# Optimization experiments

Hardware: AMD Instinct MI355X
Metric: run time of the kernel (lower is better)

The kernel has to match this reference:

```python
import jax, jax.numpy as jnp
import numpy as np

B, S, D, H = 2, 2048, 1024, 16
HD = D // H
E, K = 4, 2              # n_routed_experts, num_experts_per_tok
HID = int(4.0 * D)       # mlp_ratio * d_model
ALPHA = 0.01             # aux (load-balance) loss coefficient
EPS = 1e-5


def _ln(x, g, b):
    m = jnp.mean(x, -1, keepdims=True)
    v = jnp.var(x, -1, keepdims=True)
    return (x - m) * jax.lax.rsqrt(v + EPS) * g + b


def setup_inputs() -> dict:
    key = jax.random.key(0)
    ks = jax.random.split(key, 9)
    s = 0.02
    f32 = jnp.float32
    return {
        "x": jax.random.normal(ks[0], (B, S, D), f32),
        "ln1_g": jnp.ones((D,), f32), "ln1_b": jnp.zeros((D,), f32),
        "Wqkv": jax.random.normal(ks[1], (3 * D, D), f32) * s,
        "bqkv": jnp.zeros((3 * D,), f32),
        "Wo": jax.random.normal(ks[2], (D, D), f32) * s,
        "bo": jnp.zeros((D,), f32),
        "ln2_g": jnp.ones((D,), f32), "ln2_b": jnp.zeros((D,), f32),
        "Wg": jax.random.normal(ks[3], (E, D), f32) * s,            # router (no bias)
        "We_up": jax.random.normal(ks[4], (E, HID, D), f32) * s,
        "be_up": jnp.zeros((E, HID), f32),
        "We_down": jax.random.normal(ks[5], (E, D, HID), f32) * s,
        "be_down": jnp.zeros((E, D), f32),
        "Ws_up": jax.random.normal(ks[6], (HID, D), f32) * s,       # shared expert
        "bs_up": jnp.zeros((HID,), f32),
        "Ws_down": jax.random.normal(ks[7], (D, HID), f32) * s,
        "bs_down": jnp.zeros((D,), f32),
    }


def reference(x, ln1_g, ln1_b, Wqkv, bqkv, Wo, bo, ln2_g, ln2_b,
              Wg, We_up, be_up, We_down, be_down,
              Ws_up, bs_up, Ws_down, bs_down):
    # ---- causal multi-head self-attention (pre-LN) ----
    h = _ln(x, ln1_g, ln1_b)
    qkv = h @ Wqkv.T + bqkv                              # [B,S,3D]
    q, k, v = jnp.split(qkv, 3, axis=-1)
    to_heads = lambda t: t.reshape(B, S, H, HD).transpose(0, 2, 1, 3)
    q, k, v = to_heads(q), to_heads(k), to_heads(v)       # [B,H,S,HD]
    scores = jnp.einsum('bhqd,bhkd->bhqk', q, k) / np.float32(np.sqrt(HD))
    causal = jnp.tril(jnp.ones((S, S), bool))
    scores = jnp.where(causal, scores, jnp.float32(-1e9))
    attn = jax.nn.softmax(scores, axis=-1)
    o = jnp.einsum('bhqk,bhkd->bhqd', attn, v)
    o = o.transpose(0, 2, 1, 3).reshape(B, S, D)
    x = x + (o @ Wo.T + bo)                               # residual 1

    # ---- MoE feed-forward (pre-LN) ----
    T = B * S
    h2 = _ln(x, ln2_g, ln2_b).reshape(T, D)
    logits = h2 @ Wg.T                                    # [T,E]
    probs = jax.nn.softmax(logits, axis=-1)
    topw, topi = jax.lax.top_k(probs, K)                  # [T,K]
    topw = topw / jnp.sum(topw, -1, keepdims=True)        # renormalize top-k

    # dense expert evaluation (faithful math; kernel target is the sparse dispatch)
    up = jax.nn.gelu(jnp.einsum('td,ehd->eth', h2, We_up) + be_up[:, None, :])
    eo = jnp.einsum('eth,edh->etd', up, We_down) + be_down[:, None, :]  # [E,T,D]
    gathered = eo[topi.T, jnp.arange(T)[None, :]]         # [K,T,D]
    y = jnp.einsum('kt,ktd->td', topw.T, gathered)        # combine

    # shared expert (always-on)
    y = y + (jax.nn.gelu(h2 @ Ws_up.T + bs_up) @ Ws_down.T + bs_down)

    # load-balancing auxiliary loss (switch-style)
    assign = jax.nn.one_hot(topi, E, dtype=probs.dtype).sum(1)  # [T,E]
    fi = jnp.mean(assign, 0) / K                          # fraction routed to each expert
    Pi = jnp.mean(probs, 0)                               # mean router prob
    aux = ALPHA * E * jnp.sum(fi * Pi)

    x = x + y.reshape(B, S, D)                            # residual 2
    return aux, x
```

## Files before the change

kernel.cpp:

```cpp
#include <hip/hip_runtime.h>
#include <hip/hip_bf16.h>

#define T_TOK 4096
#define DIM   1024
#define NHEAD 16
#define HDIM  64
#define SEQ   2048
#define NEXP  4
#define HIDD  4096
#define QS    66

typedef short bf16x8 __attribute__((ext_vector_type(8)));
typedef float f32x4  __attribute__((ext_vector_type(4)));

enum { GF_GELU = 1, GF_RESID = 2, GF_SCALE = 4, GF_ACCUM = 8 };

__device__ inline unsigned short f2bf(float f) {
  union { float f; unsigned u; } v; v.f = f;
  unsigned r = v.u + 0x7FFFu + ((v.u >> 16) & 1u);
  return (unsigned short)(r >> 16);
}
__device__ inline int pack2(float a, float b) {
  return (int)((unsigned)f2bf(a) | ((unsigned)f2bf(b) << 16));
}
__device__ inline float gelu_f(float x) {
  float u = 1.5957691216057308f * x * (1.0f + 0.044715f * x * x);
  float w = __expf(u);
  return x - x * __builtin_amdgcn_rcpf(w + 1.0f);
}
__device__ inline void gld_lds16(const unsigned short* g, unsigned short* l) {
  __builtin_amdgcn_global_load_lds(
      (const __attribute__((address_space(1))) void*)g,
      (__attribute__((address_space(3))) void*)l, 16, 0, 0);
}

__global__ __launch_bounds__(256) void cvt_kernel(
    const float* __restrict__ in, unsigned short* __restrict__ out, int n8)
{
  int i = blockIdx.x * 256 + threadIdx.x;
  if (i >= n8) return;
  const float4* p = (const float4*)in + (size_t)i * 2;
  float4 v0 = p[0], v1 = p[1];
  int4 pk = make_int4(pack2(v0.x, v0.y), pack2(v0.z, v0.w),
                      pack2(v1.x, v1.y), pack2(v1.z, v1.w));
  *(int4*)(out + (size_t)i * 8) = pk;
}

__global__ __launch_bounds__(512, 2) void gemm256(
    const unsigned short* __restrict__ A, const unsigned short* __restrict__ W,
    const float* __restrict__ bias, const float* __restrict__ scale,
    unsigned short* __restrict__ C2, int N, int Kd, int flags)
{
  __shared__ __align__(16) unsigned short Abuf[2][2][256 * 32];
  __shared__ __align__(16) unsigned short Bbuf[2][2][256 * 32];

  const int tid  = threadIdx.x;
  const int wave = tid >> 6, lane = tid & 63;

  const int nwg  = gridDim.x * gridDim.y;
  const int flat = blockIdx.y * gridDim.x + blockIdx.x;
  const int swz  = (flat & 7) * (nwg >> 3) + (flat >> 3);
  const int bn = swz % gridDim.x, bm = swz / gridDim.x;

  const int sr = lane >> 2;
  const int sc = lane & 3;
  const int gcol = (sc ^ (sr & 3)) << 3;
  const unsigned short* Ag = A + ((size_t)(bm * 256 + wave * 32 + sr)) * Kd + gcol;
  const unsigned short* Wg = W + ((size_t)(bn * 256 + wave * 32 + sr)) * Kd + gcol;

  const int wm = wave >> 2, wn = wave & 3;
  const int fr = lane & 15, fq = lane >> 4;
  const int fx = (fq ^ (fr & 3)) << 3;

  f32x4 acc[8][4] = {};
  const int NT = Kd / 64;

  {
    const unsigned short* a0 = Ag;
    const unsigned short* b0 = Wg;
    gld_lds16(a0,           &Abuf[0][0][(wave * 32) * 32]);
    gld_lds16(a0 + 16 * Kd, &Abuf[0][0][(wave * 32 + 16) * 32]);
    gld_lds16(b0,           &Bbuf[0][0][(wave * 32) * 32]);
    gld_lds16(b0 + 16 * Kd, &Bbuf[0][0][(wave * 32 + 16) * 32]);
    gld_lds16(a0 + 32,           &Abuf[0][1][(wave * 32) * 32]);
    gld_lds16(a0 + 32 + 16 * Kd, &Abuf[0][1][(wave * 32 + 16) * 32]);
    gld_lds16(b0 + 32,           &Bbuf[0][1][(wave * 32) * 32]);
    gld_lds16(b0 + 32 + 16 * Kd, &Bbuf[0][1][(wave * 32 + 16) * 32]);
  }

  for (int t = 0; t < NT; ++t) {
    const int buf = t & 1, nb = buf ^ 1;
    const bool more = (t + 1 < NT);
    const int nk0 = (t + 1) * 64;
    bf16x8 a[8], b0, b1;

    asm volatile("s_waitcnt vmcnt(4)" ::: "memory");
    __builtin_amdgcn_s_barrier();
#pragma unroll
    for (int m = 0; m < 8; ++m)
      a[m] = *(const bf16x8*)&Abuf[buf][0][(wm * 128 + m * 16 + fr) * 32 + fx];
    b0 = *(const bf16x8*)&Bbuf[buf][0][(wn * 64 +  0 + fr) * 32 + fx];
    b1 = *(const bf16x8*)&Bbuf[buf][0][(wn * 64 + 16 + fr) * 32 + fx];
    if (more) {
      const unsigned short* s0 = Ag + nk0;
      gld_lds16(s0,           &Abuf[nb][0][(wave * 32) * 32]);
      gld_lds16(s0 + 16 * Kd, &Abuf[nb][0][(wave * 32 + 16) * 32]);
    }
    __builtin_amdgcn_s_setprio(1);
#pragma unroll
    for (int m = 0; m < 8; ++m) {
      acc[m][0] = __builtin_amdgcn_mfma_f32_16x16x32_bf16(a[m], b0, acc[m][0], 0, 0, 0);
      acc[m][1] = __builtin_amdgcn_mfma_f32_16x16x32_bf16(a[m], b1, acc[m][1], 0, 0, 0);
    }
    __builtin_amdgcn_s_setprio(0);

    b0 = *(const bf16x8*)&Bbuf[buf][0][(wn * 64 + 32 + fr) * 32 + fx];
    b1 = *(const bf16x8*)&Bbuf[buf][0][(wn * 64 + 48 + fr) * 32 + fx];
    if (more) {
      const unsigned short* s0 = Wg + nk0;
      gld_lds16(s0,           &Bbuf[nb][0][(wave * 32) * 32]);
      gld_lds16(s0 + 16 * Kd, &Bbuf[nb][0][(wave * 32 + 16) * 32]);
    }
    __builtin_amdgcn_s_setprio(1);
#pragma unroll
    for (int m = 0; m < 8; ++m) {
      acc[m][2] = __builtin_amdgcn_mfma_f32_16x16x32_bf16(a[m], b0, acc[m][2], 0, 0, 0);
      acc[m][3] = __builtin_amdgcn_mfma_f32_16x16x32_bf16(a[m], b1, acc[m][3], 0, 0, 0);
    }
    __builtin_amdgcn_s_setprio(0);

    asm volatile("s_waitcnt vmcnt(4)" ::: "memory");
    __builtin_amdgcn_s_barrier();
#pragma unroll
    for (int m = 0; m < 8; ++m)
      a[m] = *(const bf16x8*)&Abuf[buf][1][(wm * 128 + m * 16 + fr) * 32 + fx];
    b0 = *(const bf16x8*)&Bbuf[buf][1][(wn * 64 +  0 + fr) * 32 + fx];
    b1 = *(const bf16x8*)&Bbuf[buf][1][(wn * 64 + 16 + fr) * 32 + fx];
    if (more) {
      const unsigned short* s0 = Ag + nk0 + 32;
      gld_lds16(s0,           &Abuf[nb][1][(wave * 32) * 32]);
      gld_lds16(s0 + 16 * Kd, &Abuf[nb][1][(wave * 32 + 16) * 32]);
    }
    __builtin_amdgcn_s_setprio(1);
#pragma unroll
    for (int m = 0; m < 8; ++m) {
      acc[m][0] = __builtin_amdgcn_mfma_f32_16x16x32_bf16(a[m], b0, acc[m][0], 0, 0, 0);
      acc[m][1] = __builtin_amdgcn_mfma_f32_16x16x32_bf16(a[m], b1, acc[m][1], 0, 0, 0);
    }
    __builtin_amdgcn_s_setprio(0);

    b0 = *(const bf16x8*)&Bbuf[buf][1][(wn * 64 + 32 + fr) * 32 + fx];
    b1 = *(const bf16x8*)&Bbuf[buf][1][(wn * 64 + 48 + fr) * 32 + fx];
    if (more) {
      const unsigned short* s0 = Wg + nk0 + 32;
      gld_lds16(s0,           &Bbuf[nb][1][(wave * 32) * 32]);
      gld_lds16(s0 + 16 * Kd, &Bbuf[nb][1][(wave * 32 + 16) * 32]);
    }
    __builtin_amdgcn_s_setprio(1);
#pragma unroll
    for (int m = 0; m < 8; ++m) {
      acc[m][2] = __builtin_amdgcn_mfma_f32_16x16x32_bf16(a[m], b0, acc[m][2], 0, 0, 0);
      acc[m][3] = __builtin_amdgcn_mfma_f32_16x16x32_bf16(a[m], b1, acc[m][3], 0, 0, 0);
    }
    __builtin_amdgcn_s_setprio(0);
  }

#pragma unroll
  for (int m = 0; m < 8; ++m)
#pragma unroll
    for (int n = 0; n < 4; ++n)
#pragma unroll
      for (int r = 0; r < 4; ++r) {
        int row = bm * 256 + wm * 128 + m * 16 + fq * 4 + r;
        int col = bn * 256 + wn * 64 + n * 16 + fr;
        float v = acc[m][n][r] + bias[col];
        if (flags & GF_GELU) v = gelu_f(v);
        if (flags & GF_SCALE) v *= scale[row];
        C2[(size_t)row * N + col] = f2bf(v);
      }
}

__global__ __launch_bounds__(256) void gemm_bf16(
    const unsigned short* __restrict__ A, const unsigned short* __restrict__ W,
    const float* __restrict__ bias, const float* __restrict__ resid,
    const float* __restrict__ scale, float* __restrict__ C,
    float* __restrict__ Cz, unsigned short* __restrict__ C2,
    int M, int N, int Kd, int flags)
{
  __shared__ __align__(16) unsigned short As[128 * 64];
  __shared__ __align__(16) unsigned short Bs[128 * 64];

  const int tid  = threadIdx.x;
  const int wave = tid >> 6, lane = tid & 63;
  const int bm = blockIdx.y, bn = blockIdx.x;
  const int kz = blockIdx.z;
  const int kseg = Kd / gridDim.z;
  if (kz == 1) C = Cz;

  const int srow = lane >> 3;
  const int scol = ((lane & 7) ^ srow) << 3;
  const unsigned short* Ag = A + (size_t)(bm * 128 + wave * 32 + srow) * Kd + scol + (size_t)kz * kseg;
  const unsigned short* Wg = W + (size_t)(bn * 128 + wave * 32 + srow) * Kd + scol + (size_t)kz * kseg;
  unsigned short* AsBase = As + wave * 32 * 64;
  unsigned short* BsBase = Bs + wave * 32 * 64;

  const int wm = wave >> 1, wn = wave & 1;
  const int fr = lane & 15;
  const int fq = lane >> 4;
  const int f7 = fr & 7;

  f32x4 acc[4][4] = {};

  for (int k0 = 0; k0 < kseg; k0 += 64) {
    __syncthreads();
    gld_lds16(Ag + k0,            AsBase);
    gld_lds16(Ag + k0 +  8 * Kd,  AsBase +  8 * 64);
    gld_lds16(Ag + k0 + 16 * Kd,  AsBase + 16 * 64);
    gld_lds16(Ag + k0 + 24 * Kd,  AsBase + 24 * 64);
    gld_lds16(Wg + k0,            BsBase);
    gld_lds16(Wg + k0 +  8 * Kd,  BsBase +  8 * 64);
    gld_lds16(Wg + k0 + 16 * Kd,  BsBase + 16 * 64);
    gld_lds16(Wg + k0 + 24 * Kd,  BsBase + 24 * 64);
    __syncthreads();
#pragma unroll
    for (int ks = 0; ks < 2; ++ks) {
      const int ch = ((ks * 4 + fq) ^ f7) << 3;
      bf16x8 a[4], b[4];
#pragma unroll
      for (int i = 0; i < 4; ++i) {
        a[i] = *(const bf16x8*)&As[(wm * 64 + i * 16 + fr) * 64 + ch];
        b[i] = *(const bf16x8*)&Bs[(wn * 64 + i * 16 + fr) * 64 + ch];
      }
#pragma unroll
      for (int mt = 0; mt < 4; ++mt)
#pragma unroll
        for (int nt = 0; nt < 4; ++nt)
          acc[mt][nt] = __builtin_amdgcn_mfma_f32_16x16x32_bf16(a[mt], b[nt], acc[mt][nt], 0, 0, 0);
    }
  }

#pragma unroll
  for (int mt = 0; mt < 4; ++mt)
#pragma unroll
    for (int nt = 0; nt < 4; ++nt)
#pragma unroll
      for (int r = 0; r < 4; ++r) {
        int row = bm * 128 + wm * 64 + mt * 16 + fq * 4 + r;
        int col = bn * 128 + wn * 64 + nt * 16 + fr;
        float v = acc[mt][nt][r];
        if (bias) v += bias[col];
        if (flags & GF_GELU) v = gelu_f(v);
        if (flags & GF_RESID) v += resid[(size_t)row * N + col];
        if (flags & GF_SCALE) v *= scale[row];
        size_t idx = (size_t)row * N + col;
        if (C) { if (flags & GF_ACCUM) C[idx] += v; else C[idx] = v; }
        if (C2) C2[idx] = f2bf(v);
      }
}

__global__ __launch_bounds__(256) void attn_mfma(
    const unsigned short* __restrict__ qkv, unsigned short* __restrict__ o)
{
  __shared__ __align__(16) unsigned short Qs[64 * QS];
  __shared__ __align__(16) unsigned short Ks[64 * QS];
  __shared__ __align__(16) unsigned short Vt[64 * QS];
  __shared__ __align__(16) unsigned short Ps[64 * QS];

  const int tid  = threadIdx.x;
  const int wave = tid >> 6, lane = tid & 63;
  const int quad = lane >> 4, l15 = lane & 15;
  const int bh = blockIdx.y, b = bh >> 4, h = bh & 15;

  const int srow = tid >> 2;
  const int scol = (tid & 3) << 4;
  const int swcol = srow ^ ((tid & 3) << 3);

  const unsigned short* kvb = qkv + (size_t)b * SEQ * 3072 + 1024 + h * 64 + scol;

  int4 ka, kb, va, vb;

  for (int half = 0; half < 2; ++half) {
    const int qb = half ? (31 - (int)blockIdx.x) : (int)blockIdx.x;
    const int q0 = qb << 6;

    __syncthreads();
    {
      const unsigned short* qp = qkv + ((size_t)(b * SEQ + q0 + srow)) * 3072 + h * 64 + scol;
      *(int4*)&Qs[srow * QS + scol]     = *(const int4*)qp;
      *(int4*)&Qs[srow * QS + scol + 8] = *(const int4*)(qp + 8);
    }
    {
      const unsigned short* kp = kvb + (size_t)srow * 3072;
      ka = *(const int4*)kp;           kb = *(const int4*)(kp + 8);
      va = *(const int4*)(kp + 1024);  vb = *(const int4*)(kp + 1024 + 8);
    }
    __syncthreads();
    bf16x8 qf0 = *(const bf16x8*)&Qs[(wave * 16 + l15) * QS + quad * 8];
    bf16x8 qf1 = *(const bf16x8*)&Qs[(wave * 16 + l15) * QS + 32 + quad * 8];

    f32x4 Oc[4] = {};
    float mr[4] = {-1e30f, -1e30f, -1e30f, -1e30f};
    float ls[4] = {0.f, 0.f, 0.f, 0.f};

    for (int kt = 0; kt <= qb; ++kt) {
      __syncthreads();
      {
        *(int4*)&Ks[srow * QS + scol]     = ka;
        *(int4*)&Ks[srow * QS + scol + 8] = kb;
        unsigned short vs[16];
        *(int4*)&vs[0] = va;
        *(int4*)&vs[8] = vb;
#pragma unroll
        for (int i = 0; i < 16; ++i)
          Vt[(scol + i) * QS + swcol] = vs[i];
      }
      if (kt < qb) {
        const unsigned short* kp = kvb + (size_t)((kt + 1) * 64 + srow) * 3072;
        ka = *(const int4*)kp;           kb = *(const int4*)(kp + 8);
        va = *(const int4*)(kp + 1024);  vb = *(const int4*)(kp + 1024 + 8);
      }
      __syncthreads();

      f32x4 sc[4] = {};
#pragma unroll
      for (int ct = 0; ct < 4; ++ct) {
        bf16x8 k0 = *(const bf16x8*)&Ks[(ct * 16 + l15) * QS + quad * 8];
        bf16x8 k1 = *(const bf16x8*)&Ks[(ct * 16 + l15) * QS + 32 + quad * 8];
        sc[ct] = __builtin_amdgcn_mfma_f32_16x16x32_bf16(qf0, k0, sc[ct], 0, 0, 0);
        sc[ct] = __builtin_amdgcn_mfma_f32_16x16x32_bf16(qf1, k1, sc[ct], 0, 0, 0);
      }

      float sv[4][4];
      const bool diag = (kt == qb);
#pragma unroll
      for (int ct = 0; ct < 4; ++ct)
#pragma unroll
        for (int r = 0; r < 4; ++r) {
          float v = sc[ct][r] * 0.125f;
          if (diag && (ct * 16 + l15) > (wave * 16 + quad * 4 + r)) v = -1e9f;
          sv[ct][r] = v;
        }
      float rm[4], rs[4];
#pragma unroll
      for (int r = 0; r < 4; ++r)
        rm[r] = fmaxf(fmaxf(sv[0][r], sv[1][r]), fmaxf(sv[2][r], sv[3][r]));
#pragma unroll
      for (int m = 1; m < 16; m <<= 1)
#pragma unroll
        for (int r = 0; r < 4; ++r) rm[r] = fmaxf(rm[r], __shfl_xor(rm[r], m, 16));
      float al[4];
#pragma unroll
      for (int r = 0; r < 4; ++r) {
        float nm = fmaxf(mr[r], rm[r]);
        al[r] = __expf(mr[r] - nm);
        mr[r] = nm;
        rs[r] = 0.f;
      }
#pragma unroll
      for (int ct = 0; ct < 4; ++ct)
#pragma unroll
        for (int r = 0; r < 4; ++r) {
          float p = __expf(sv[ct][r] - mr[r]);
          sv[ct][r] = p;
          rs[r] += p;
        }
#pragma unroll
      for (int m = 1; m < 16; m <<= 1)
#pragma unroll
        for (int r = 0; r < 4; ++r) rs[r] += __shfl_xor(rs[r], m, 16);
#pragma unroll
      for (int r = 0; r < 4; ++r) {
        ls[r] = ls[r] * al[r] + rs[r];
        for (int ct = 0; ct < 4; ++ct) Oc[ct][r] *= al[r];
      }
#pragma unroll
      for (int ct = 0; ct < 4; ++ct)
#pragma unroll
        for (int r = 0; r < 4; ++r)
          Ps[(wave * 16 + quad * 4 + r) * QS + ct * 16 + l15] = f2bf(sv[ct][r]);
      bf16x8 pf0 = *(const bf16x8*)&Ps[(wave * 16 + l15) * QS + quad * 8];
      bf16x8 pf1 = *(const bf16x8*)&Ps[(wave * 16 + l15) * QS + 32 + quad * 8];
#pragma unroll
      for (int ct = 0; ct < 4; ++ct) {
        bf16x8 v0 = *(const bf16x8*)&Vt[(ct * 16 + l15) * QS + ((quad ^ ct) << 3)];
        bf16x8 v1 = *(const bf16x8*)&Vt[(ct * 16 + l15) * QS + 32 + ((quad ^ ct) << 3)];
        Oc[ct] = __builtin_amdgcn_mfma_f32_16x16x32_bf16(pf0, v0, Oc[ct], 0, 0, 0);
        Oc[ct] = __builtin_amdgcn_mfma_f32_16x16x32_bf16(pf1, v1, Oc[ct], 0, 0, 0);
      }
    }

#pragma unroll
    for (int r = 0; r < 4; ++r) {
      float inv = 1.0f / ls[r];
      unsigned short* orow = o + ((size_t)(b * SEQ + q0 + wave * 16 + quad * 4 + r)) * DIM + h * 64;
#pragma unroll
      for (int ct = 0; ct < 4; ++ct)
        orow[ct * 16 + l15] = f2bf(Oc[ct][r] * inv);
    }
  }
}

__global__ __launch_bounds__(256) void ln_kernel(
    const float* __restrict__ x, const float* __restrict__ g,
    const float* __restrict__ b, unsigned short* __restrict__ out)
{
  const int t = blockIdx.x, tid = threadIdx.x;
  const float* row = x + (size_t)t * DIM;
  float4 v = *(const float4*)(row + tid * 4);
  float s  = v.x + v.y + v.z + v.w;
  float s2 = v.x * v.x + v.y * v.y + v.z * v.z + v.w * v.w;
  for (int off = 1; off < 64; off <<= 1) {
    s  += __shfl_xor(s, off, 64);
    s2 += __shfl_xor(s2, off, 64);
  }
  __shared__ float red[8];
  const int wave = tid >> 6, lane = tid & 63;
  if (lane == 0) { red[wave] = s; red[4 + wave] = s2; }
  __syncthreads();
  float S  = red[0] + red[1] + red[2] + red[3];
  float S2 = red[4] + red[5] + red[6] + red[7];
  float mean = S * (1.0f / DIM);
  float var  = S2 * (1.0f / DIM) - mean * mean;
  float rstd = rsqrtf(var + 1e-5f);
  float4 gv = *(const float4*)(g + tid * 4);
  float4 bv = *(const float4*)(b + tid * 4);
  float ox = (v.x - mean) * rstd * gv.x + bv.x;
  float oy = (v.y - mean) * rstd * gv.y + bv.y;
  float oz = (v.z - mean) * rstd * gv.z + bv.z;
  float ow = (v.w - mean) * rstd * gv.w + bv.w;
  int2 pk; pk.x = pack2(ox, oy); pk.y = pack2(oz, ow);
  *(int2*)(out + (size_t)t * DIM + tid * 4) = pk;
}

__global__ __launch_bounds__(128) void router_kernel(
    const float* __restrict__ xin, const float* __restrict__ g,
    const float* __restrict__ bb, const float* __restrict__ Wgp,
    float* __restrict__ stab, float* __restrict__ probs4, int* __restrict__ tops)
{
  const int t = blockIdx.x, tid = threadIdx.x;
  const float* row = xin + (size_t)t * DIM;
  float v[8]; float s = 0.f, s2 = 0.f;
#pragma unroll
  for (int k = 0; k < 8; ++k) {
    float u = row[tid + 128 * k];
    v[k] = u; s += u; s2 += u * u;
  }
  for (int off = 1; off < 64; off <<= 1) {
    s  += __shfl_xor(s, off, 64);
    s2 += __shfl_xor(s2, off, 64);
  }
  __shared__ float red[4];
  const int wv = tid >> 6, ln = tid & 63;
  if (ln == 0) { red[wv] = s; red[2 + wv] = s2; }
  __syncthreads();
  float S = red[0] + red[1], S2 = red[2] + red[3];
  float mean = S * (1.0f / DIM);
  float var  = S2 * (1.0f / DIM) - mean * mean;
  float rstd = rsqrtf(var + 1e-5f);
  float p0 = 0, p1 = 0, p2 = 0, p3 = 0;
#pragma unroll
  for (int k = 0; k < 8; ++k) {
    int i = tid + 128 * k;
    float hv = (v[k] - mean) * rstd * g[i] + bb[i];
    p0 += hv * Wgp[i];
    p1 += hv * Wgp[DIM + i];
    p2 += hv * Wgp[2 * DIM + i];
    p3 += hv * Wgp[3 * DIM + i];
  }
  __shared__ float sm[4][128];
  sm[0][tid] = p0; sm[1][tid] = p1; sm[2][tid] = p2; sm[3][tid] = p3;
  __syncthreads();
  for (int sft = 64; sft > 0; sft >>= 1) {
    if (tid < sft)
      for (int e = 0; e < 4; ++e) sm[e][tid] += sm[e][tid + sft];
    __syncthreads();
  }
  if (tid == 0) {
    float l[4] = { sm[0][0], sm[1][0], sm[2][0], sm[3][0] };
    float m = fmaxf(fmaxf(l[0], l[1]), fmaxf(l[2], l[3]));
    float pr[4]; float sum = 0.f;
    for (int e = 0; e < 4; ++e) { pr[e] = __expf(l[e] - m); sum += pr[e]; }
    for (int e = 0; e < 4; ++e) pr[e] /= sum;
    int i0 = 0;
    for (int e = 1; e < 4; ++e) if (pr[e] > pr[i0]) i0 = e;
    int i1 = -1;
    for (int e = 0; e < 4; ++e) if (e != i0 && (i1 < 0 || pr[e] > pr[i1])) i1 = e;
    float wsum = pr[i0] + pr[i1];
    for (int e = 0; e < 4; ++e)
      stab[(size_t)e * T_TOK + t] = (e == i0) ? pr[i0] / wsum : (e == i1) ? pr[i1] / wsum : 0.f;
    ((float4*)probs4)[t] = make_float4(pr[0], pr[1], pr[2], pr[3]);
    tops[t] = i0 | (i1 << 2);
  }
}

__global__ __launch_bounds__(256) void moe_stats_kernel(
    const float* __restrict__ probs4, const int* __restrict__ tops,
    float* __restrict__ outaux)
{
  const int tid = threadIdx.x;
  float pi0 = 0, pi1 = 0, pi2 = 0, pi3 = 0;
  float fi0 = 0, fi1 = 0, fi2 = 0, fi3 = 0;
  for (int t = tid; t < T_TOK; t += 256) {
    float4 p = ((const float4*)probs4)[t];
    pi0 += p.x; pi1 += p.y; pi2 += p.z; pi3 += p.w;
    int ii = tops[t];
    int a = ii & 3, b = (ii >> 2) & 3;
    fi0 += (a == 0 ? 1.f : 0.f) + (b == 0 ? 1.f : 0.f);
    fi1 += (a == 1 ? 1.f : 0.f) + (b == 1 ? 1.f : 0.f);
    fi2 += (a == 2 ? 1.f : 0.f) + (b == 2 ? 1.f : 0.f);
    fi3 += (a == 3 ? 1.f : 0.f) + (b == 3 ? 1.f : 0.f);
  }
  for (int off = 1; off < 64; off <<= 1) {
    pi0 += __shfl_xor(pi0, off, 64); pi1 += __shfl_xor(pi1, off, 64);
    pi2 += __shfl_xor(pi2, off, 64); pi3 += __shfl_xor(pi3, off, 64);
    fi0 += __shfl_xor(fi0, off, 64); fi1 += __shfl_xor(fi1, off, 64);
    fi2 += __shfl_xor(fi2, off, 64); fi3 += __shfl_xor(fi3, off, 64);
  }
  __shared__ float red[8][4];
  const int wv = tid >> 6, ln = tid & 63;
  if (ln == 0) {
    red[0][wv] = pi0; red[1][wv] = pi1; red[2][wv] = pi2; red[3][wv] = pi3;
    red[4][wv] = fi0; red[5][wv] = fi1; red[6][wv] = fi2; red[7][wv] = fi3;
  }
  __syncthreads();
  if (tid == 0) {
    float P[4], F[4];
    for (int e = 0; e < 4; ++e) {
      P[e] = red[e][0] + red[e][1] + red[e][2] + red[e][3];
      F[e] = red[4 + e][0] + red[4 + e][1] + red[4 + e][2] + red[4 + e][3];
    }
    float sacc = F[0] * P[0] + F[1] * P[1] + F[2] * P[2] + F[3] * P[3];
    outaux[0] = 0.01f * 4.0f * sacc / (2.0f * (float)T_TOK * (float)T_TOK);
  }
}

__global__ __launch_bounds__(256) void init_y_kernel(
    const float* __restrict__ bs_dn, const float* __restrict__ be_dn,
    const float* __restrict__ stab, float* __restrict__ y, float* __restrict__ y2)
{
  const int t = blockIdx.x, c = threadIdx.x;
  float s0 = stab[t], s1 = stab[T_TOK + t], s2 = stab[2 * T_TOK + t], s3 = stab[3 * T_TOK + t];
  float4 acc = ((const float4*)bs_dn)[c];
  float4 b0 = ((const float4*)(be_dn + 0 * DIM))[c];
  float4 b1 = ((const float4*)(be_dn + 1 * DIM))[c];
  float4 b2 = ((const float4*)(be_dn + 2 * DIM))[c];
  float4 b3 = ((const float4*)(be_dn + 3 * DIM))[c];
  acc.x += s0 * b0.x + s1 * b1.x + s2 * b2.x + s3 * b3.x;
  acc.y += s0 * b0.y + s1 * b1.y + s2 * b2.y + s3 * b3.y;
  acc.z += s0 * b0.z + s1 * b1.z + s2 * b2.z + s3 * b3.z;
  acc.w += s0 * b0.w + s1 * b1.w + s2 * b2.w + s3 * b3.w;
  ((float4*)(y + (size_t)t * DIM))[c] = acc;
  ((float4*)(y2 + (size_t)t * DIM))[c] = make_float4(0.f, 0.f, 0.f, 0.f);
}

__global__ __launch_bounds__(256) void add3_kernel(
    const float* __restrict__ a, const float* __restrict__ b,
    const float* __restrict__ c, float* __restrict__ out, int n)
{
  int i = blockIdx.x * 256 + threadIdx.x;
  if (i < n) out[i] = a[i] + b[i] + c[i];
}

extern "C" void kernel_launch(void* const* d_in, const int* in_sizes, int n_in,
                              void* d_out, int out_size, void* d_ws, size_t ws_size,
                              hipStream_t stream)
{
  const float* x      = (const float*)d_in[0];
  const float* ln1_g  = (const float*)d_in[1];
  const float* ln1_b  = (const float*)d_in[2];
  const float* Wqkv   = (const float*)d_in[3];
  const float* bqkv   = (const float*)d_in[4];
  const float* Wo     = (const float*)d_in[5];
  const float* bo     = (const float*)d_in[6];
  const float* ln2_g  = (const float*)d_in[7];
  const float* ln2_b  = (const float*)d_in[8];
  const float* Wg     = (const float*)d_in[9];
  const float* We_up  = (const float*)d_in[10];
  const float* be_up  = (const float*)d_in[11];
  const float* We_dn  = (const float*)d_in[12];
  const float* be_dn  = (const float*)d_in[13];
  const float* Ws_up  = (const float*)d_in[14];
  const float* bs_up  = (const float*)d_in[15];
  const float* Ws_dn  = (const float*)d_in[16];
  const float* bs_dn  = (const float*)d_in[17];

  float* out = (float*)d_out;
  const size_t TD = (size_t)T_TOK * DIM;

  char* w = (char*)d_ws;
  float* x1 = (float*)w;  w += TD * 4;
  float* y  = (float*)w;
  unsigned short* o_bf = (unsigned short*)y;
  w += TD * 4;
  float* y2 = (float*)w;  w += TD * 4;
  unsigned short* pool = (unsigned short*)w;
  unsigned short* qkv_bf = pool;
  unsigned short* up_bf  = pool;
  w += (size_t)T_TOK * HIDD * 2;
  unsigned short* h_bf = (unsigned short*)w;  w += TD * 2;
  unsigned short* P1   = (unsigned short*)w;  w += (size_t)HIDD * DIM * 2;
  unsigned short* P2   = (unsigned short*)w;  w += (size_t)HIDD * DIM * 2;
  float* stab = (float*)w;  w += (size_t)NEXP * T_TOK * 4;
  float* probs4 = (float*)w; w += (size_t)T_TOK * 4 * 4;
  int*   tops   = (int*)w;   w += (size_t)T_TOK * 4;

  auto cvt = [&](const float* src, unsigned short* dst, int n) {
    cvt_kernel<<<(n / 8 + 255) / 256, 256, 0, stream>>>(src, dst, n / 8);
  };

  cvt(Wqkv, P1, 3 * DIM * DIM);
  ln_kernel<<<T_TOK, 256, 0, stream>>>(x, ln1_g, ln1_b, h_bf);
  gemm256<<<dim3(3072 / 256, T_TOK / 256), 512, 0, stream>>>(
      h_bf, P1, bqkv, nullptr, qkv_bf, 3072, DIM, 0);
  attn_mfma<<<dim3(16, 2 * NHEAD), 256, 0, stream>>>(qkv_bf, o_bf);
  cvt(Wo, P2, DIM * DIM);
  gemm_bf16<<<dim3(DIM / 128, T_TOK / 128), 256, 0, stream>>>(
      o_bf, P2, bo, x, nullptr, x1, nullptr, nullptr, T_TOK, DIM, DIM, GF_RESID);
  ln_kernel<<<T_TOK, 256, 0, stream>>>(x1, ln2_g, ln2_b, h_bf);
  router_kernel<<<T_TOK, 128, 0, stream>>>(x1, ln2_g, ln2_b, Wg, stab, probs4, tops);
  moe_stats_kernel<<<1, 256, 0, stream>>>(probs4, tops, out);
  init_y_kernel<<<T_TOK, 256, 0, stream>>>(bs_dn, be_dn, stab, y, y2);
  cvt(Ws_up, P1, HIDD * DIM);
  gemm256<<<dim3(HIDD / 256, T_TOK / 256), 512, 0, stream>>>(
      h_bf, P1, bs_up, nullptr, up_bf, HIDD, DIM, GF_GELU);
  cvt(Ws_dn, P2, DIM * HIDD);
  gemm_bf16<<<dim3(DIM / 128, T_TOK / 128, 2), 256, 0, stream>>>(
      up_bf, P2, nullptr, nullptr, nullptr, y, y2, nullptr, T_TOK, DIM, HIDD, GF_ACCUM);
  for (int e = 0; e < NEXP; ++e) {
    cvt(We_up + (size_t)e * HIDD * DIM, P1, HIDD * DIM);
    gemm256<<<dim3(HIDD / 256, T_TOK / 256), 512, 0, stream>>>(
        h_bf, P1, be_up + (size_t)e * HIDD, stab + (size_t)e * T_TOK, up_bf,
        HIDD, DIM, GF_GELU | GF_SCALE);
    cvt(We_dn + (size_t)e * DIM * HIDD, P2, DIM * HIDD);
    gemm_bf16<<<dim3(DIM / 128, T_TOK / 128, 2), 256, 0, stream>>>(
        up_bf, P2, nullptr, nullptr, nullptr, y, y2, nullptr,
        T_TOK, DIM, HIDD, GF_ACCUM);
  }
  add3_kernel<<<(int)(TD / 256), 256, 0, stream>>>(x1, y, y2, out + 1, (int)TD);
}
```

Before: 1.038 ms.

## Use split-K gemm256 with atomic accumulation for down projections; unpair attention blocks

Adds split-K support and an fp32 atomicAdd epilogue to the 256x256 MFMA GEMM. All five down-projection GEMMs now use it with a 4-way K split, replacing the smaller 128-tile GEMM and its two-buffer (y/y2) split-K accumulation. This removes the y2 buffer, its zeroing, and one operand of the final add. Attention now launches one block per query tile (32 per head) instead of pairing a light and a heavy tile in one block. That adds parallelism but loses the built-in load balancing. Atomics add memory traffic and make the summation order nondeterministic.

After: 1.247 ms. 1.2x slower.

```diff
diff --git a/kernel.cpp b/kernel.cpp
--- a/kernel.cpp
+++ b/kernel.cpp
@@ -49,7 +49,8 @@
 __global__ __launch_bounds__(512, 2) void gemm256(
     const unsigned short* __restrict__ A, const unsigned short* __restrict__ W,
     const float* __restrict__ bias, const float* __restrict__ scale,
-    unsigned short* __restrict__ C2, int N, int Kd, int flags)
+    unsigned short* __restrict__ C2, float* __restrict__ Cacc,
+    int N, int Kd, int flags)
 {
   __shared__ __align__(16) unsigned short Abuf[2][2][256 * 32];
   __shared__ __align__(16) unsigned short Bbuf[2][2][256 * 32];
@@ -62,18 +63,21 @@
   const int swz  = (flat & 7) * (nwg >> 3) + (flat >> 3);
   const int bn = swz % gridDim.x, bm = swz / gridDim.x;
 
+  const int kz   = blockIdx.z;
+  const int kseg = Kd / gridDim.z;
+  const int NT   = kseg / 64;
+
   const int sr = lane >> 2;
   const int sc = lane & 3;
   const int gcol = (sc ^ (sr & 3)) << 3;
-  const unsigned short* Ag = A + ((size_t)(bm * 256 + wave * 32 + sr)) * Kd + gcol;
-  const unsigned short* Wg = W + ((size_t)(bn * 256 + wave * 32 + sr)) * Kd + gcol;
+  const unsigned short* Ag = A + ((size_t)(bm * 256 + wave * 32 + sr)) * Kd + gcol + (size_t)kz * kseg;
+  const unsigned short* Wg = W + ((size_t)(bn * 256 + wave * 32 + sr)) * Kd + gcol + (size_t)kz * kseg;
 
   const int wm = wave >> 2, wn = wave & 3;
   const int fr = lane & 15, fq = lane >> 4;
   const int fx = (fq ^ (fr & 3)) << 3;
 
   f32x4 acc[8][4] = {};
-  const int NT = Kd / 64;
 
   {
     const unsigned short* a0 = Ag;
@@ -173,10 +177,13 @@
       for (int r = 0; r < 4; ++r) {
         int row = bm * 256 + wm * 128 + m * 16 + fq * 4 + r;
         int col = bn * 256 + wn * 64 + n * 16 + fr;
-        float v = acc[m][n][r] + bias[col];
+        float v = acc[m][n][r];
+        if (bias) v += bias[col];
         if (flags & GF_GELU) v = gelu_f(v);
         if (flags & GF_SCALE) v *= scale[row];
-        C2[(size_t)row * N + col] = f2bf(v);
+        size_t idx = (size_t)row * N + col;
+        if (Cacc) atomicAdd(&Cacc[idx], v);
+        else      C2[idx] = f2bf(v);
       }
 }
 
@@ -277,126 +284,123 @@
 
   const unsigned short* kvb = qkv + (size_t)b * SEQ * 3072 + 1024 + h * 64 + scol;
 
+  const int qb = 31 - (int)blockIdx.x;
+  const int q0 = qb << 6;
+
   int4 ka, kb, va, vb;
 
-  for (int half = 0; half < 2; ++half) {
-    const int qb = half ? (31 - (int)blockIdx.x) : (int)blockIdx.x;
-    const int q0 = qb << 6;
-
+  {
+    const unsigned short* qp = qkv + ((size_t)(b * SEQ + q0 + srow)) * 3072 + h * 64 + scol;
+    *(int4*)&Qs[srow * QS + scol]     = *(const int4*)qp;
+    *(int4*)&Qs[srow * QS + scol + 8] = *(const int4*)(qp + 8);
+  }
+  {
+    const unsigned short* kp = kvb + (size_t)srow * 3072;
+    ka = *(const int4*)kp;           kb = *(const int4*)(kp + 8);
+    va = *(const int4*)(kp + 1024);  vb = *(const int4*)(kp + 1024 + 8);
+  }
+  __syncthreads();
+  bf16x8 qf0 = *(const bf16x8*)&Qs[(wave * 16 + l15) * QS + quad * 8];
+  bf16x8 qf1 = *(const bf16x8*)&Qs[(wave * 16 + l15) * QS + 32 + quad * 8];
+
+  f32x4 Oc[4] = {};
+  float mr[4] = {-1e30f, -1e30f, -1e30f, -1e30f};
+  float ls[4] = {0.f, 0.f, 0.f, 0.f};
+
+  for (int kt = 0; kt <= qb; ++kt) {
     __syncthreads();
     {
-      const unsigned short* qp = qkv + ((size_t)(b * SEQ + q0 + srow)) * 3072 + h * 64 + scol;
-      *(int4*)&Qs[srow * QS + scol]     = *(const int4*)qp;
-      *(int4*)&Qs[srow * QS + scol + 8] = *(const int4*)(qp + 8);
-    }
-    {
-      const unsigned short* kp = kvb + (size_t)srow * 3072;
+      *(int4*)&Ks[srow * QS + scol]     = ka;
+      *(int4*)&Ks[srow * QS + scol + 8] = kb;
+      unsigned short vs[16];
+      *(int4*)&vs[0] = va;
+      *(int4*)&vs[8] = vb;
+#pragma unroll
+      for (int i = 0; i < 16; ++i)
+        Vt[(scol + i) * QS + swcol] = vs[i];
+    }
+    if (kt < qb) {
+      const unsigned short* kp = kvb + (size_t)((kt + 1) * 64 + srow) * 3072;
       ka = *(const int4*)kp;           kb = *(const int4*)(kp + 8);
       va = *(const int4*)(kp + 1024);  vb = *(const int4*)(kp + 1024 + 8);
     }
     __syncthreads();
-    bf16x8 qf0 = *(const bf16x8*)&Qs[(wave * 16 + l15) * QS + quad * 8];
-    bf16x8 qf1 = *(const bf16x8*)&Qs[(wave * 16 + l15) * QS + 32 + quad * 8];
-
-    f32x4 Oc[4] = {};
-    float mr[4] = {-1e30f, -1e30f, -1e30f, -1e30f};
-    float ls[4] = {0.f, 0.f, 0.f, 0.f};
-
-    for (int kt = 0; kt <= qb; ++kt) {
-      __syncthreads();
-      {
-        *(int4*)&Ks[srow * QS + scol]     = ka;
-        *(int4*)&Ks[srow * QS + scol + 8] = kb;
-        unsigned short vs[16];
-        *(int4*)&vs[0] = va;
-        *(int4*)&vs[8] = vb;
-#pragma unroll
-        for (int i = 0; i < 16; ++i)
-          Vt[(scol + i) * QS + swcol] = vs[i];
+
+    f32x4 sc[4] = {};
+#pragma unroll
+    for (int ct = 0; ct < 4; ++ct) {
+      bf16x8 k0 = *(const bf16x8*)&Ks[(ct * 16 + l15) * QS + quad * 8];
+      bf16x8 k1 = *(const bf16x8*)&Ks[(ct * 16 + l15) * QS + 32 + quad * 8];
+      sc[ct] = __builtin_amdgcn_mfma_f32_16x16x32_bf16(qf0, k0, sc[ct], 0, 0, 0);
+      sc[ct] = __builtin_amdgcn_mfma_f32_16x16x32_bf16(qf1, k1, sc[ct], 0, 0, 0);
+    }
+
+    float sv[4][4];
+    const bool diag = (kt == qb);
+#pragma unroll
+    for (int ct = 0; ct < 4; ++ct)
+#pragma unroll
+      for (int r = 0; r < 4; ++r) {
+        float v = sc[ct][r] * 0.125f;
+        if (diag && (ct * 16 + l15) > (wave * 16 + quad * 4 + r)) v = -1e9f;
+        sv[ct][r] = v;
       }
-      if (kt < qb) {
-        const unsigned short* kp = kvb + (size_t)((kt + 1) * 64 + srow) * 3072;
-        ka = *(const int4*)kp;           kb = *(const int4*)(kp + 8);
-        va = *(const int4*)(kp + 1024);  vb = *(const int4*)(kp + 1024 + 8);
+    float rm[4], rs[4];
+#pragma unroll
+    for (int r = 0; r < 4; ++r)
+      rm[r] = fmaxf(fmaxf(sv[0][r], sv[1][r]), fmaxf(sv[2][r], sv[3][r]));
+#pragma unroll
+    for (int m = 1; m < 16; m <<= 1)
+#pragma unroll
+      for (int r = 0; r < 4; ++r) rm[r] = fmaxf(rm[r], __shfl_xor(rm[r], m, 16));
+    float al[4];
+#pragma unroll
+    for (int r = 0; r < 4; ++r) {
+      float nm = fmaxf(mr[r], rm[r]);
+      al[r] = __expf(mr[r] - nm);
+      mr[r] = nm;
+      rs[r] = 0.f;
+    }
+#pragma unroll
+    for (int ct = 0; ct < 4; ++ct)
+#pragma unroll
+      for (int r = 0; r < 4; ++r) {
+        float p = __expf(sv[ct][r] - mr[r]);
+        sv[ct][r] = p;
+        rs[r] += p;
       }
-      __syncthreads();
-
-      f32x4 sc[4] = {};
-#pragma unroll
-      for (int ct = 0; ct < 4; ++ct) {
-        bf16x8 k0 = *(const bf16x8*)&Ks[(ct * 16 + l15) * QS + quad * 8];
-        bf16x8 k1 = *(const bf16x8*)&Ks[(ct * 16 + l15) * QS + 32 + quad * 8];
-        sc[ct] = __builtin_amdgcn_mfma_f32_16x16x32_bf16(qf0, k0, sc[ct], 0, 0, 0);
-        sc[ct] = __builtin_amdgcn_mfma_f32_16x16x32_bf16(qf1, k1, sc[ct], 0, 0, 0);
-      }
-
-      float sv[4][4];
-      const bool diag = (kt == qb);
-#pragma unroll
-      for (int ct = 0; ct < 4; ++ct)
-#pragma unroll
-        for (int r = 0; r < 4; ++r) {
-          float v = sc[ct][r] * 0.125f;
-          if (diag && (ct * 16 + l15) > (wave * 16 + quad * 4 + r)) v = -1e9f;
-          sv[ct][r] = v;
-        }
-      float rm[4], rs[4];
+#pragma unroll
+    for (int m = 1; m < 16; m <<= 1)
+#pragma unroll
+      for (int r = 0; r < 4; ++r) rs[r] += __shfl_xor(rs[r], m, 16);
+#pragma unroll
+    for (int r = 0; r < 4; ++r) {
+      ls[r] = ls[r] * al[r] + rs[r];
+      for (int ct = 0; ct < 4; ++ct) Oc[ct][r] *= al[r];
+    }
+#pragma unroll
+    for (int ct = 0; ct < 4; ++ct)
 #pragma unroll
       for (int r = 0; r < 4; ++r)
-        rm[r] = fmaxf(fmaxf(sv[0][r], sv[1][r]), fmaxf(sv[2][r], sv[3][r]));
-#pragma unroll
-      for (int m = 1; m < 16; m <<= 1)
-#pragma unroll
-        for (int r = 0; r < 4; ++r) rm[r] = fmaxf(rm[r], __shfl_xor(rm[r], m, 16));
-      float al[4];
-#pragma unroll
-      for (int r = 0; r < 4; ++r) {
-        float nm = fmaxf(mr[r], rm[r]);
-        al[r] = __expf(mr[r] - nm);
-        mr[r] = nm;
-        rs[r] = 0.f;
-      }
-#pragma unroll
-      for (int ct = 0; ct < 4; ++ct)
-#pragma unroll
-        for (int r = 0; r < 4; ++r) {
-          float p = __expf(sv[ct][r] - mr[r]);
-          sv[ct][r] = p;
-          rs[r] += p;
-        }
-#pragma unroll
-      for (int m = 1; m < 16; m <<= 1)
-#pragma unroll
-        for (int r = 0; r < 4; ++r) rs[r] += __shfl_xor(rs[r], m, 16);
-#pragma unroll
-      for (int r = 0; r < 4; ++r) {
-        ls[r] = ls[r] * al[r] + rs[r];
-        for (int ct = 0; ct < 4; ++ct) Oc[ct][r] *= al[r];
-      }
-#pragma unroll
-      for (int ct = 0; ct < 4; ++ct)
-#pragma unroll
-        for (int r = 0; r < 4; ++r)
-          Ps[(wave * 16 + quad * 4 + r) * QS + ct * 16 + l15] = f2bf(sv[ct][r]);
-      bf16x8 pf0 = *(const bf16x8*)&Ps[(wave * 16 + l15) * QS + quad * 8];
-      bf16x8 pf1 = *(const bf16x8*)&Ps[(wave * 16 + l15) * QS + 32 + quad * 8];
-#pragma unroll
-      for (int ct = 0; ct < 4; ++ct) {
-        bf16x8 v0 = *(const bf16x8*)&Vt[(ct * 16 + l15) * QS + ((quad ^ ct) << 3)];
-        bf16x8 v1 = *(const bf16x8*)&Vt[(ct * 16 + l15) * QS + 32 + ((quad ^ ct) << 3)];
-        Oc[ct] = __builtin_amdgcn_mfma_f32_16x16x32_bf16(pf0, v0, Oc[ct], 0, 0, 0);
-        Oc[ct] = __builtin_amdgcn_mfma_f32_16x16x32_bf16(pf1, v1, Oc[ct], 0, 0, 0);
-      }
-    }
-
-#pragma unroll
-    for (int r = 0; r < 4; ++r) {
-      float inv = 1.0f / ls[r];
-      unsigned short* orow = o + ((size_t)(b * SEQ + q0 + wave * 16 + quad * 4 + r)) * DIM + h * 64;
-#pragma unroll
-      for (int ct = 0; ct < 4; ++ct)
-        orow[ct * 16 + l15] = f2bf(Oc[ct][r] * inv);
-    }
+        Ps[(wave * 16 + quad * 4 + r) * QS + ct * 16 + l15] = f2bf(sv[ct][r]);
+    bf16x8 pf0 = *(const bf16x8*)&Ps[(wave * 16 + l15) * QS + quad * 8];
+    bf16x8 pf1 = *(const bf16x8*)&Ps[(wave * 16 + l15) * QS + 32 + quad * 8];
+#pragma unroll
+    for (int ct = 0; ct < 4; ++ct) {
+      bf16x8 v0 = *(const bf16x8*)&Vt[(ct * 16 + l15) * QS + ((quad ^ ct) << 3)];
+      bf16x8 v1 = *(const bf16x8*)&Vt[(ct * 16 + l15) * QS + 32 + ((quad ^ ct) << 3)];
+      Oc[ct] = __builtin_amdgcn_mfma_f32_16x16x32_bf16(pf0, v0, Oc[ct], 0, 0, 0);
+      Oc[ct] = __builtin_amdgcn_mfma_f32_16x16x32_bf16(pf1, v1, Oc[ct], 0, 0, 0);
+    }
+  }
+
+#pragma unroll
+  for (int r = 0; r < 4; ++r) {
+    float inv = 1.0f / ls[r];
+    unsigned short* orow = o + ((size_t)(b * SEQ + q0 + wave * 16 + quad * 4 + r)) * DIM + h * 64;
+#pragma unroll
+    for (int ct = 0; ct < 4; ++ct)
+      orow[ct * 16 + l15] = f2bf(Oc[ct][r] * inv);
   }
 }
 
@@ -536,7 +540,7 @@
 
 __global__ __launch_bounds__(256) void init_y_kernel(
     const float* __restrict__ bs_dn, const float* __restrict__ be_dn,
-    const float* __restrict__ stab, float* __restrict__ y, float* __restrict__ y2)
+    const float* __restrict__ stab, float* __restrict__ y)
 {
   const int t = blockIdx.x, c = threadIdx.x;
   float s0 = stab[t], s1 = stab[T_TOK + t], s2 = stab[2 * T_TOK + t], s3 = stab[3 * T_TOK + t];
@@ -550,15 +554,14 @@
   acc.z += s0 * b0.z + s1 * b1.z + s2 * b2.z + s3 * b3.z;
   acc.w += s0 * b0.w + s1 * b1.w + s2 * b2.w + s3 * b3.w;
   ((float4*)(y + (size_t)t * DIM))[c] = acc;
-  ((float4*)(y2 + (size_t)t * DIM))[c] = make_float4(0.f, 0.f, 0.f, 0.f);
-}
-
-__global__ __launch_bounds__(256) void add3_kernel(
+}
+
+__global__ __launch_bounds__(256) void add2_kernel(
     const float* __restrict__ a, const float* __restrict__ b,
-    const float* __restrict__ c, float* __restrict__ out, int n)
+    float* __restrict__ out, int n)
 {
   int i = blockIdx.x * 256 + threadIdx.x;
-  if (i < n) out[i] = a[i] + b[i] + c[i];
+  if (i < n) out[i] = a[i] + b[i];
 }
 
 extern "C" void kernel_launch(void* const* d_in, const int* in_sizes, int n_in,
@@ -592,7 +595,6 @@
   float* y  = (float*)w;
   unsigned short* o_bf = (unsigned short*)y;
   w += TD * 4;
-  float* y2 = (float*)w;  w += TD * 4;
   unsigned short* pool = (unsigned short*)w;
   unsigned short* qkv_bf = pool;
   unsigned short* up_bf  = pool;
@@ -611,30 +613,29 @@
   cvt(Wqkv, P1, 3 * DIM * DIM);
   ln_kernel<<<T_TOK, 256, 0, stream>>>(x, ln1_g, ln1_b, h_bf);
   gemm256<<<dim3(3072 / 256, T_TOK / 256), 512, 0, stream>>>(
-      h_bf, P1, bqkv, nullptr, qkv_bf, 3072, DIM, 0);
-  attn_mfma<<<dim3(16, 2 * NHEAD), 256, 0, stream>>>(qkv_bf, o_bf);
+      h_bf, P1, bqkv, nullptr, qkv_bf, nullptr, 3072, DIM, 0);
+  attn_mfma<<<dim3(32, 2 * NHEAD), 256, 0, stream>>>(qkv_bf, o_bf);
   cvt(Wo, P2, DIM * DIM);
   gemm_bf16<<<dim3(DIM / 128, T_TOK / 128), 256, 0, stream>>>(
       o_bf, P2, bo, x, nullptr, x1, nullptr, nullptr, T_TOK, DIM, DIM, GF_RESID);
   ln_kernel<<<T_TOK, 256, 0, stream>>>(x1, ln2_g, ln2_b, h_bf);
   router_kernel<<<T_TOK, 128, 0, stream>>>(x1, ln2_g, ln2_b, Wg, stab, probs4, tops);
   moe_stats_kernel<<<1, 256, 0, stream>>>(probs4, tops, out);
-  init_y_kernel<<<T_TOK, 256, 0, stream>>>(bs_dn, be_dn, stab, y, y2);
+  init_y_kernel<<<T_TOK, 256, 0, stream>>>(bs_dn, be_dn, stab, y);
   cvt(Ws_up, P1, HIDD * DIM);
   gemm256<<<dim3(HIDD / 256, T_TOK / 256), 512, 0, stream>>>(
-      h_bf, P1, bs_up, nullptr, up_bf, HIDD, DIM, GF_GELU);
+      h_bf, P1, bs_up, nullptr, up_bf, nullptr, HIDD, DIM, GF_GELU);
   cvt(Ws_dn, P2, DIM * HIDD);
-  gemm_bf16<<<dim3(DIM / 128, T_TOK / 128, 2), 256, 0, stream>>>(
-      up_bf, P2, nullptr, nullptr, nullptr, y, y2, nullptr, T_TOK, DIM, HIDD, GF_ACCUM);
+  gemm256<<<dim3(DIM / 256, T_TOK / 256, 4), 512, 0, stream>>>(
+      up_bf, P2, nullptr, nullptr, nullptr, y, DIM, HIDD, 0);
   for (int e = 0; e < NEXP; ++e) {
     cvt(We_up + (size_t)e * HIDD * DIM, P1, HIDD * DIM);
     gemm256<<<dim3(HIDD / 256, T_TOK / 256), 512, 0, stream>>>(
         h_bf, P1, be_up + (size_t)e * HIDD, stab + (size_t)e * T_TOK, up_bf,
-        HIDD, DIM, GF_GELU | GF_SCALE);
+        nullptr, HIDD, DIM, GF_GELU | GF_SCALE);
     cvt(We_dn + (size_t)e * DIM * HIDD, P2, DIM * HIDD);
-    gemm_bf16<<<dim3(DIM / 128, T_TOK / 128, 2), 256, 0, stream>>>(
-        up_bf, P2, nullptr, nullptr, nullptr, y, y2, nullptr,
-        T_TOK, DIM, HIDD, GF_ACCUM);
-  }
-  add3_kernel<<<(int)(TD / 256), 256, 0, stream>>>(x1, y, y2, out + 1, (int)TD);
-}
+    gemm256<<<dim3(DIM / 256, T_TOK / 256, 4), 512, 0, stream>>>(
+        up_bf, P2, nullptr, nullptr, nullptr, y, DIM, HIDD, 0);
+  }
+  add2_kernel<<<(int)(TD / 256), 256, 0, stream>>>(x1, y, out + 1, (int)TD);
+}
```
